# Performance work log

Hardware: AMD Instinct MI355X
Metric: run time of the kernel (lower is better)

Reference implementation:

```python
import jax, jax.numpy as jnp
import numpy as np

B, O, I = 128, 1024, 1024
EPS = 1e-07

def setup_inputs() -> dict:
    key = jax.random.key(0)
    ks = jax.random.split(key, 7)
    data = jax.random.normal(ks[0], (B, I), dtype=jnp.float32)
    # parameters, matching torch init: 2*rand-1, rand+0.1, 2*rand-1, ones+0.1, rand, rand
    input_x = 2.0 * jax.random.uniform(ks[1], (1, O, I), dtype=jnp.float32) - 1.0
    input_y = jax.random.uniform(ks[2], (1, O, I), dtype=jnp.float32) + 0.1
    output_x = 2.0 * jax.random.uniform(ks[3], (1, O, I), dtype=jnp.float32) - 1.0
    output_y = jnp.ones((1, O, I), dtype=jnp.float32) + 0.1
    linkage_add = jax.random.uniform(ks[4], (1, O, I), dtype=jnp.float32)
    linkage_mul = jax.random.uniform(ks[5], (1, O, I), dtype=jnp.float32)
    return {"data": data, "input_x": input_x, "input_y": input_y,
            "output_x": output_x, "output_y": output_y,
            "linkage_add": linkage_add, "linkage_mul": linkage_mul}

def reference(data, input_x, input_y, output_x, output_y, linkage_add, linkage_mul):
    shape = data.shape
    d = data.reshape(-1, 1, I)                      # (B,1,I)
    inp = input_x / input_y                          # (1,O,I)
    out = output_x / output_y                        # (1,O,I)
    tests = (inp + linkage_add) * (1.0 + linkage_mul)
    error = (tests - out) * jax.nn.sigmoid(d)        # (B,O,I)
    w = jax.nn.softmax(1.0 / jnp.sqrt(error * error + EPS), axis=1)
    expect = d * w                                   # (B,O,I)
    return jnp.sum(expect, axis=2).reshape(shape)
```

## Files before the change

### kernel.cpp

```cpp
#include <hip/hip_runtime.h>

#define B_ 128
#define O_ 1024
#define I_ 1024
#define NCHUNK 64
#define CI (I_ / NCHUNK)
#define WPB 4
#define TT_BYTES ((size_t)O_ * I_ * sizeof(float))

#define LOG2E_F  1.4426950408889634f
#define LN2_F    0.6931471805599453f
#define LN2SQ_F  0.4804530139182014f
#define EPSC_F   (1e-7f * LN2SQ_F)

typedef float v2f __attribute__((ext_vector_type(2)));

__device__ __forceinline__ float fast_rsq(float x)  { return __builtin_amdgcn_rsqf(x); }
__device__ __forceinline__ float fast_exp2(float x) { return __builtin_amdgcn_exp2f(x); }
__device__ __forceinline__ float fast_rcp(float x)  { return __builtin_amdgcn_rcpf(x); }

__global__ __launch_bounds__(256) void build_T2_kernel(
    const float* __restrict__ ix, const float* __restrict__ iy,
    const float* __restrict__ ox, const float* __restrict__ oy,
    const float* __restrict__ la, const float* __restrict__ lm,
    float* __restrict__ Tt2)
{
    __shared__ float tile[32][33];
    const int i0 = blockIdx.x * 32;
    const int o0 = blockIdx.y * 32;
    const int tx = threadIdx.x;
    const int ty = threadIdx.y;

#pragma unroll
    for (int r = 0; r < 32; r += 8) {
        const int o = o0 + ty + r;
        const int i = i0 + tx;
        const int idx = o * I_ + i;
        const float t = fmaf(ix[idx] * fast_rcp(iy[idx]) + la[idx],
                             1.0f + lm[idx],
                             -(ox[idx] * fast_rcp(oy[idx])));
        tile[ty + r][tx] = t * t;
    }
    __syncthreads();
#pragma unroll
    for (int r = 0; r < 32; r += 8) {
        const int i = i0 + ty + r;
        const int o = o0 + tx;
        Tt2[i * O_ + o] = tile[tx][ty + r];
    }
}

__global__ __launch_bounds__(64) void min_row_kernel(
    const float* __restrict__ Tt2, float* __restrict__ minr2)
{
    const int i = blockIdx.x;
    const int lane = threadIdx.x;
    const float4* row = (const float4*)(Tt2 + (size_t)i * O_);
    float mn = 3.4e38f;
#pragma unroll
    for (int k = 0; k < 4; ++k) {
        const float4 v = row[lane + 64 * k];
        mn = fminf(mn, fminf(fminf(v.x, v.y), fminf(v.z, v.w)));
    }
#pragma unroll
    for (int off = 32; off > 0; off >>= 1)
        mn = fminf(mn, __shfl_xor(mn, off));
    if (lane == 0) minr2[i] = mn;
}

__global__ __launch_bounds__(256) void aeg_main_kernel(
    const float* __restrict__ data,
    const float* __restrict__ Tt2,
    const float* __restrict__ minr2,
    float* __restrict__ out)
{
    __shared__ float red[WPB][O_];

    const int w    = threadIdx.x >> 6;
    const int lane = threadIdx.x & 63;
    const int chunk = blockIdx.x * WPB + w;
    const int b     = blockIdx.y;

    const float* dptr = data + b * I_ + chunk * CI;
    const float4* rowbase = (const float4*)(Tt2 + (size_t)chunk * CI * O_);

    v2f acc2[8];
#pragma unroll
    for (int j = 0; j < 8; ++j) acc2[j] = (v2f)0.0f;

    auto load_row = [&](float4 (&r)[4], int ii) {
        const float4* row = rowbase + (size_t)ii * (O_ / 4);
#pragma unroll
        for (int k = 0; k < 4; ++k) r[k] = row[lane + 64 * k];
    };

    auto body = [&](const float4 (&r)[4], int ii) {
        const float dv = dptr[ii];
        const float sig = fast_rcp(1.0f + fast_exp2(-dv * LOG2E_F));
        const float sigc = sig * LN2_F;
        const float s2 = sigc * sigc;

        float mr2;
        if (minr2) {
            mr2 = minr2[chunk * CI + ii];
        } else {
            float mn = 3.4e38f;
#pragma unroll
            for (int k = 0; k < 4; ++k)
                mn = fminf(mn, fminf(fminf(r[k].x, r[k].y), fminf(r[k].z, r[k].w)));
#pragma unroll
            for (int off = 32; off > 0; off >>= 1)
                mn = fminf(mn, __shfl_xor(mn, off));
            mr2 = mn;
        }
        const float m2 = fast_rsq(fmaf(mr2, s2, EPSC_F));

        const v2f s2v = {s2, s2};
        const v2f epv = {EPSC_F, EPSC_F};
        const v2f m2v = {m2, m2};

        v2f e2[8];
        v2f zv = (v2f)0.0f;
#pragma unroll
        for (int k = 0; k < 4; ++k) {
            const v2f a = {r[k].x, r[k].y};
            const v2f c = {r[k].z, r[k].w};
            const v2f q0 = a * s2v + epv;
            const v2f q1 = c * s2v + epv;
            v2f t0, t1;
            t0.x = fast_rsq(q0.x); t0.y = fast_rsq(q0.y);
            t1.x = fast_rsq(q1.x); t1.y = fast_rsq(q1.y);
            t0 -= m2v;
            t1 -= m2v;
            v2f ev0, ev1;
            ev0.x = fast_exp2(t0.x); ev0.y = fast_exp2(t0.y);
            ev1.x = fast_exp2(t1.x); ev1.y = fast_exp2(t1.y);
            e2[2 * k]     = ev0;
            e2[2 * k + 1] = ev1;
            zv += ev0;
            zv += ev1;
        }
        float z = zv.x + zv.y;
#pragma unroll
        for (int off = 32; off > 0; off >>= 1)
            z += __shfl_xor(z, off);

        const float scale = dv * fast_rcp(z);
        const v2f sc = {scale, scale};
#pragma unroll
        for (int j = 0; j < 8; ++j)
            acc2[j] = e2[j] * sc + acc2[j];
    };

    float4 rA[4], rB[4];
    load_row(rA, 0);
    for (int ii = 0; ii < CI; ii += 2) {
        load_row(rB, ii + 1);
        body(rA, ii);
        if (ii + 2 < CI) load_row(rA, ii + 2);
        body(rB, ii + 1);
    }

#pragma unroll
    for (int k = 0; k < 4; ++k) {
        float4 v;
        v.x = acc2[2 * k].x;     v.y = acc2[2 * k].y;
        v.z = acc2[2 * k + 1].x; v.w = acc2[2 * k + 1].y;
        ((float4*)&red[w][256 * k])[lane] = v;
    }
    __syncthreads();

    const int t = threadIdx.x;
    float4 v = ((const float4*)red[0])[t];
#pragma unroll
    for (int ww = 1; ww < WPB; ++ww) {
        const float4 u = ((const float4*)red[ww])[t];
        v.x += u.x; v.y += u.y; v.z += u.z; v.w += u.w;
    }
    float* ob = out + b * O_ + 4 * t;
    atomicAdd(&ob[0], v.x);
    atomicAdd(&ob[1], v.y);
    atomicAdd(&ob[2], v.z);
    atomicAdd(&ob[3], v.w);
}

extern "C" void kernel_launch(void* const* d_in, const int* in_sizes, int n_in,
                              void* d_out, int out_size, void* d_ws, size_t ws_size,
                              hipStream_t stream)
{
    const float* data = (const float*)d_in[0];
    const float* ix   = (const float*)d_in[1];
    const float* iy   = (const float*)d_in[2];
    const float* ox   = (const float*)d_in[3];
    const float* oy   = (const float*)d_in[4];
    const float* la   = (const float*)d_in[5];
    const float* lm   = (const float*)d_in[6];
    float* out  = (float*)d_out;
    float* Tt2  = (float*)d_ws;
    float* minr2 = (ws_size >= TT_BYTES + I_ * sizeof(float))
                       ? (float*)((char*)d_ws + TT_BYTES) : nullptr;

    hipMemsetAsync(d_out, 0, (size_t)B_ * O_ * sizeof(float), stream);

    build_T2_kernel<<<dim3(I_ / 32, O_ / 32), dim3(32, 8), 0, stream>>>(
        ix, iy, ox, oy, la, lm, Tt2);

    if (minr2)
        min_row_kernel<<<I_, 64, 0, stream>>>(Tt2, minr2);

    aeg_main_kernel<<<dim3(NCHUNK / WPB, B_), 256, 0, stream>>>(
        data, Tt2, minr2, out);
}
```

Before: 130.0 us.

## Fuse row-min and output zeroing into build kernel, hoist per-row scalars, DPP reductions

The row-minimum pass is folded into the transpose/build kernel using shared and global atomicMin on float bits, which is valid because every value is a non-negative square. The output zeroing also moves into that kernel, so the separate min kernel and the output memset are gone, leaving one small memset for the min buffer. The main kernel precomputes sigmoid, scale and max terms for all 16 rows up front with vector loads made wave-uniform via readfirstlane. It also replaces the shuffle-based wave sum with a DPP reduction plus readlane and fully unrolls the row loop with double-buffered loads. This assumes the workspace always holds the min buffer and adds register pressure from the unrolled per-row arrays.

```diff
diff --git a/kernel.cpp b/kernel.cpp
--- a/kernel.cpp
+++ b/kernel.cpp
@@ -19,27 +19,57 @@
 __device__ __forceinline__ float fast_exp2(float x) { return __builtin_amdgcn_exp2f(x); }
 __device__ __forceinline__ float fast_rcp(float x)  { return __builtin_amdgcn_rcpf(x); }
 
+__device__ __forceinline__ float rfl(float x) {
+    return __builtin_bit_cast(float,
+        __builtin_amdgcn_readfirstlane(__builtin_bit_cast(int, x)));
+}
+
+template <int CTRL>
+__device__ __forceinline__ float dpp_add(float v) {
+    int x = __builtin_amdgcn_update_dpp(0, __builtin_bit_cast(int, v),
+                                        CTRL, 0xf, 0xf, true);
+    return v + __builtin_bit_cast(float, x);
+}
+__device__ __forceinline__ float wave_sum_uniform(float v) {
+    v = dpp_add<0xB1>(v);
+    v = dpp_add<0x4E>(v);
+    v = dpp_add<0x141>(v);
+    v = dpp_add<0x140>(v);
+    v = dpp_add<0x142>(v);
+    v = dpp_add<0x143>(v);
+    return __builtin_bit_cast(float,
+        __builtin_amdgcn_readlane(__builtin_bit_cast(int, v), 63));
+}
+
 __global__ __launch_bounds__(256) void build_T2_kernel(
     const float* __restrict__ ix, const float* __restrict__ iy,
     const float* __restrict__ ox, const float* __restrict__ oy,
     const float* __restrict__ la, const float* __restrict__ lm,
-    float* __restrict__ Tt2)
+    float* __restrict__ Tt2, unsigned* __restrict__ minbits,
+    float* __restrict__ out_zero)
 {
     __shared__ float tile[32][33];
+    __shared__ unsigned mloc[32];
     const int i0 = blockIdx.x * 32;
     const int o0 = blockIdx.y * 32;
     const int tx = threadIdx.x;
     const int ty = threadIdx.y;
+    const int t  = ty * 32 + tx;
+
+    if (t < 32) mloc[t] = 0xFFFFFFFFu;
+
+    const int bid = blockIdx.y * gridDim.x + blockIdx.x;
+    if (t < 128) out_zero[bid * 128 + t] = 0.0f;
 
 #pragma unroll
     for (int r = 0; r < 32; r += 8) {
         const int o = o0 + ty + r;
         const int i = i0 + tx;
         const int idx = o * I_ + i;
-        const float t = fmaf(ix[idx] * fast_rcp(iy[idx]) + la[idx],
-                             1.0f + lm[idx],
-                             -(ox[idx] * fast_rcp(oy[idx])));
-        tile[ty + r][tx] = t * t;
+        const float tt = fmaf(ix[idx] * fast_rcp(iy[idx]) + la[idx],
+                              1.0f + lm[idx],
+                              -(ox[idx] * fast_rcp(oy[idx])));
+        tile[ty + r][tx] = tt * tt;
     }
     __syncthreads();
 #pragma unroll
@@ -48,24 +78,13 @@
         const int o = o0 + tx;
         Tt2[i * O_ + o] = tile[tx][ty + r];
     }
-}
-
-__global__ __launch_bounds__(64) void min_row_kernel(
-    const float* __restrict__ Tt2, float* __restrict__ minr2)
-{
-    const int i = blockIdx.x;
-    const int lane = threadIdx.x;
-    const float4* row = (const float4*)(Tt2 + (size_t)i * O_);
-    float mn = 3.4e38f;
-#pragma unroll
-    for (int k = 0; k < 4; ++k) {
-        const float4 v = row[lane + 64 * k];
-        mn = fminf(mn, fminf(fminf(v.x, v.y), fminf(v.z, v.w)));
-    }
-#pragma unroll
-    for (int off = 32; off > 0; off >>= 1)
-        mn = fminf(mn, __shfl_xor(mn, off));
-    if (lane == 0) minr2[i] = mn;
+    const int il = t & 31;
+    const int g  = t >> 5;
+    float mn = fminf(fminf(tile[4 * g + 0][il], tile[4 * g + 1][il]),
+                     fminf(tile[4 * g + 2][il], tile[4 * g + 3][il]));
+    atomicMin(&mloc[il], __builtin_bit_cast(unsigned, mn));
+    __syncthreads();
+    if (t < 32) atomicMin(&minbits[i0 + t], mloc[t]);
 }
 
 __global__ __launch_bounds__(256) void aeg_main_kernel(
@@ -81,46 +100,55 @@
     const int chunk = blockIdx.x * WPB + w;
     const int b     = blockIdx.y;
 
-    const float* dptr = data + b * I_ + chunk * CI;
     const float4* rowbase = (const float4*)(Tt2 + (size_t)chunk * CI * O_);
 
+    const float4* dv4 = (const float4*)(data + b * I_ + chunk * CI);
+    const float4* mr4 = (const float4*)(minr2 + chunk * CI);
+    float dvf[CI], mrf[CI];
+#pragma unroll
+    for (int k = 0; k < 4; ++k) {
+        const float4 a = dv4[k];
+        const float4 m = mr4[k];
+        dvf[4 * k + 0] = a.x; dvf[4 * k + 1] = a.y;
+        dvf[4 * k + 2] = a.z; dvf[4 * k + 3] = a.w;
+        mrf[4 * k + 0] = m.x; mrf[4 * k + 1] = m.y;
+        mrf[4 * k + 2] = m.z; mrf[4 * k + 3] = m.w;
+    }
+    float sdv[CI], ss2[CI], sm2[CI];
+#pragma unroll
+    for (int j = 0; j < CI; ++j) {
+        const float dv  = dvf[j];
+        const float sig = fast_rcp(1.0f + fast_exp2(-dv * LOG2E_F));
+        const float sc  = sig * LN2_F;
+        const float s2  = sc * sc;
+        const float m2  = fast_rsq(fmaf(mrf[j], s2, EPSC_F));
+        sdv[j] = rfl(dv);
+        ss2[j] = rfl(s2);
+        sm2[j] = rfl(m2);
+    }
+
     v2f acc2[8];
 #pragma unroll
     for (int j = 0; j < 8; ++j) acc2[j] = (v2f)0.0f;
 
-    auto load_row = [&](float4 (&r)[4], int ii) {
-        const float4* row = rowbase + (size_t)ii * (O_ / 4);
-#pragma unroll
-        for (int k = 0; k < 4; ++k) r[k] = row[lane + 64 * k];
-    };
-
-    auto body = [&](const float4 (&r)[4], int ii) {
-        const float dv = dptr[ii];
-        const float sig = fast_rcp(1.0f + fast_exp2(-dv * LOG2E_F));
-        const float sigc = sig * LN2_F;
-        const float s2 = sigc * sigc;
-
-        float mr2;
-        if (minr2) {
-            mr2 = minr2[chunk * CI + ii];
-        } else {
-            float mn = 3.4e38f;
-#pragma unroll
-            for (int k = 0; k < 4; ++k)
-                mn = fminf(mn, fminf(fminf(r[k].x, r[k].y), fminf(r[k].z, r[k].w)));
-#pragma unroll
-            for (int off = 32; off > 0; off >>= 1)
-                mn = fminf(mn, __shfl_xor(mn, off));
-            mr2 = mn;
+    float4 rr[2][4];
+#pragma unroll
+    for (int k = 0; k < 4; ++k) rr[0][k] = rowbase[lane + 64 * k];
+
+#pragma unroll
+    for (int ii = 0; ii < CI; ++ii) {
+        if (ii + 1 < CI) {
+            const float4* nrow = rowbase + (size_t)(ii + 1) * (O_ / 4);
+#pragma unroll
+            for (int k = 0; k < 4; ++k) rr[(ii + 1) & 1][k] = nrow[lane + 64 * k];
         }
-        const float m2 = fast_rsq(fmaf(mr2, s2, EPSC_F));
-
-        const v2f s2v = {s2, s2};
+        const float4* r = rr[ii & 1];
+        const v2f s2v = {ss2[ii], ss2[ii]};
+        const v2f m2v = {sm2[ii], sm2[ii]};
         const v2f epv = {EPSC_F, EPSC_F};
-        const v2f m2v = {m2, m2};
 
         v2f e2[8];
-        v2f zv = (v2f)0.0f;
+        v2f zv0 = (v2f)0.0f, zv1 = (v2f)0.0f;
 #pragma unroll
         for (int k = 0; k < 4; ++k) {
             const v2f a = {r[k].x, r[k].y};
@@ -137,28 +165,16 @@
             ev1.x = fast_exp2(t1.x); ev1.y = fast_exp2(t1.y);
             e2[2 * k]     = ev0;
             e2[2 * k + 1] = ev1;
-            zv += ev0;
-            zv += ev1;
+            zv0 += ev0;
+            zv1 += ev1;
         }
-        float z = zv.x + zv.y;
-#pragma unroll
-        for (int off = 32; off > 0; off >>= 1)
-            z += __shfl_xor(z, off);
-
-        const float scale = dv * fast_rcp(z);
-        const v2f sc = {scale, scale};
+        const v2f zv = zv0 + zv1;
+        const float zt = wave_sum_uniform(zv.x + zv.y);
+        const float scale = sdv[ii] * fast_rcp(zt);
+        const v2f sc2 = {scale, scale};
 #pragma unroll
         for (int j = 0; j < 8; ++j)
-            acc2[j] = e2[j] * sc + acc2[j];
-    };
-
-    float4 rA[4], rB[4];
-    load_row(rA, 0);
-    for (int ii = 0; ii < CI; ii += 2) {
-        load_row(rB, ii + 1);
-        body(rA, ii);
-        if (ii + 2 < CI) load_row(rA, ii + 2);
-        body(rB, ii + 1);
+            acc2[j] = e2[j] * sc2 + acc2[j];
     }
 
 #pragma unroll
@@ -197,17 +213,13 @@
     const float* lm   = (const float*)d_in[6];
     float* out  = (float*)d_out;
     float* Tt2  = (float*)d_ws;
-    float* minr2 = (ws_size >= TT_BYTES + I_ * sizeof(float))
-                       ? (float*)((char*)d_ws + TT_BYTES) : nullptr;
-
-    hipMemsetAsync(d_out, 0, (size_t)B_ * O_ * sizeof(float), stream);
+    unsigned* minbits = (unsigned*)((char*)d_ws + TT_BYTES);
+
+    (void)hipMemsetAsync(minbits, 0xFF, I_ * sizeof(unsigned), stream);
 
     build_T2_kernel<<<dim3(I_ / 32, O_ / 32), dim3(32, 8), 0, stream>>>(
-        ix, iy, ox, oy, la, lm, Tt2);
-
-    if (minr2)
-        min_row_kernel<<<I_, 64, 0, stream>>>(Tt2, minr2);
+        ix, iy, ox, oy, la, lm, Tt2, minbits, out);
 
     aeg_main_kernel<<<dim3(NCHUNK / WPB, B_), 256, 0, stream>>>(
-        data, Tt2, minr2, out);
-}
+        data, Tt2, (const float*)minbits, out);
+}
```

Measured after the change: 121.3 us. -6.7%, faster.
